# Kernel optimization log

Hardware: AMD Instinct MI355X
Metric: run time of the kernel (lower is better)

## Reference

```python
import jax, jax.numpy as jnp
import numpy as np

B, L, HID = 2, 2048, 512
NUM_HEADS = 8
HEAD_DIM = HID // NUM_HEADS
GAP_ROWS = 33   # num_time_gap_buckets + 1
DUR_ROWS = 17   # num_duration_buckets + 1
NEG = -1e9      # finite stand-in for -inf (grad-safe, masked probs ~0)


def setup_inputs() -> dict:
    key = jax.random.key(0)
    ks = jax.random.split(key, 16)
    s = 1.0 / np.sqrt(HID)
    x = jax.random.normal(ks[0], (B, L, HID), dtype=jnp.float32)
    attention_mask = jax.random.randint(ks[1], (B, L), 0, 2, dtype=jnp.int32)
    time_gap_bucket_ids = jax.random.randint(ks[2], (B, L), 0, GAP_ROWS, dtype=jnp.int32)
    duration_bucket_ids = jax.random.randint(ks[3], (B, L), 0, DUR_ROWS, dtype=jnp.int32)
    Wq = jax.random.normal(ks[4], (HID, HID), dtype=jnp.float32) * s
    bq = jnp.zeros((HID,), jnp.float32)
    Wk = jax.random.normal(ks[5], (HID, HID), dtype=jnp.float32) * s
    bk = jnp.zeros((HID,), jnp.float32)
    Wv = jax.random.normal(ks[6], (HID, HID), dtype=jnp.float32) * s
    bv = jnp.zeros((HID,), jnp.float32)
    Wo = jax.random.normal(ks[7], (HID, HID), dtype=jnp.float32) * s
    bo = jnp.zeros((HID,), jnp.float32)
    # bias tables: padding_idx=0 row kept at zero, rest random for a meaningful test
    gap_emb = jax.random.normal(ks[8], (GAP_ROWS, NUM_HEADS), dtype=jnp.float32) * 0.1
    gap_emb = gap_emb.at[0].set(0.0)
    dur_emb = jax.random.normal(ks[9], (DUR_ROWS, NUM_HEADS), dtype=jnp.float32) * 0.1
    dur_emb = dur_emb.at[0].set(0.0)
    return dict(x=x, attention_mask=attention_mask,
                time_gap_bucket_ids=time_gap_bucket_ids,
                duration_bucket_ids=duration_bucket_ids,
                Wq=Wq, bq=bq, Wk=Wk, bk=bk, Wv=Wv, bv=bv, Wo=Wo, bo=bo,
                gap_emb=gap_emb, dur_emb=dur_emb)


def reference(x, attention_mask, time_gap_bucket_ids, duration_bucket_ids,
              Wq, bq, Wk, bk, Wv, bv, Wo, bo, gap_emb, dur_emb):
    b, l, hid = x.shape
    h, d = NUM_HEADS, HEAD_DIM
    def split_heads(t):  # (B,L,HID) -> (B,h,L,d)
        return t.reshape(b, l, h, d).transpose(0, 2, 1, 3)
    Q = split_heads(x @ Wq + bq)
    K = split_heads(x @ Wk + bk)
    V = split_heads(x @ Wv + bv)
    scores = jnp.einsum('bhqd,bhkd->bhqk', Q, K) / jnp.sqrt(jnp.float32(d))
    # relative time-gap bias: (B,L,L) bucket lookup -> (B,h,L,L)
    rel = jnp.abs(time_gap_bucket_ids[:, :, None] - time_gap_bucket_ids[:, None, :])
    rel = jnp.clip(rel, 0, GAP_ROWS - 1)
    gap_bias = gap_emb[rel]                       # (B,L,L,h)
    scores = scores + gap_bias.transpose(0, 3, 1, 2)
    # per-key duration bias: (B,L,h) -> (B,h,1,L)
    dur_bias = dur_emb[duration_bucket_ids]       # (B,L,h)
    scores = scores + dur_bias.transpose(0, 2, 1)[:, :, None, :]
    pad = (attention_mask == 0)[:, None, None, :]  # (B,1,1,L) over keys
    scores = jnp.where(pad, NEG, scores)
    attn = jax.nn.softmax(scores, axis=-1)
    out = jnp.einsum('bhqk,bhkd->bhqd', attn, V)
    out = out.transpose(0, 2, 1, 3).reshape(b, l, hid)
    return out @ Wo + bo
```

## Files before the change

kernel.cpp:

```cpp
#include <hip/hip_runtime.h>
#include <cmath>

typedef unsigned short u16;
typedef unsigned int   u32;
typedef __attribute__((ext_vector_type(2))) unsigned uintx2;
typedef __attribute__((ext_vector_type(4))) float    floatx4;
typedef __attribute__((ext_vector_type(4))) unsigned uintx4;
typedef __attribute__((ext_vector_type(8))) __bf16   bf16x8;

#define MFMA16(a, b, c) __builtin_amdgcn_mfma_f32_16x16x32_bf16((a), (b), (c), 0, 0, 0)

__device__ __forceinline__ u16 f2bf(float f) {
    union { float f; u32 u; } v; v.f = f;
    u32 u = v.u;
    return (u16)((u + 0x7FFFu + ((u >> 16) & 1u)) >> 16);
}

__device__ __forceinline__ bf16x8 ld_frag(const u16* p) {
    uintx4 t = *(const uintx4*)p;
    return __builtin_bit_cast(bf16x8, t);
}

#if __has_builtin(__builtin_amdgcn_exp2f)
#define EXP2F(x) __builtin_amdgcn_exp2f(x)
#else
#define EXP2F(x) exp2f(x)
#endif

typedef __attribute__((address_space(3))) unsigned       lds_u32;
typedef __attribute__((address_space(1))) const unsigned glb_u32;
__device__ __forceinline__ void gl_lds16(const void* g, void* l) {
    __builtin_amdgcn_global_load_lds((glb_u32*)(uintptr_t)g, (lds_u32*)(uintptr_t)l, 16, 0, 0);
}

#define LOG2E   1.4426950408889634f
#define QSCALE  0.18033688011112043f

__global__ __launch_bounds__(256) void cast_x_kernel(const float* __restrict__ x,
                                                     u16* __restrict__ Xb) {
    int idx = blockIdx.x * 256 + threadIdx.x;
    const float* src = x + (size_t)idx * 8;
    uintx4 o;
    o.x = f2bf(src[0]) | ((u32)f2bf(src[1]) << 16);
    o.y = f2bf(src[2]) | ((u32)f2bf(src[3]) << 16);
    o.z = f2bf(src[4]) | ((u32)f2bf(src[5]) << 16);
    o.w = f2bf(src[6]) | ((u32)f2bf(src[7]) << 16);
    *(uintx4*)(Xb + (size_t)idx * 8) = o;
}

__global__ __launch_bounds__(256) void transpose_w_kernel(
        const float* __restrict__ Wq, const float* __restrict__ Wk,
        const float* __restrict__ Wv, const float* __restrict__ Wo,
        u16* __restrict__ WqT, u16* __restrict__ WkT,
        u16* __restrict__ WvT, u16* __restrict__ WoT) {
    int m = blockIdx.y;
    const float* W = (m == 0) ? Wq : (m == 1) ? Wk : (m == 2) ? Wv : Wo;
    u16* WT = (m == 0) ? WqT : (m == 1) ? WkT : (m == 2) ? WvT : WoT;
    int idx = blockIdx.x * 256 + threadIdx.x;
    int n = idx >> 9, k = idx & 511;
    WT[idx] = f2bf(W[(size_t)k * 512 + n]);
}

__global__ __launch_bounds__(256) void ext_q_kernel(const int* __restrict__ gap_ids,
                                                    u16* __restrict__ Qe) {
    int idx = blockIdx.x * 256 + threadIdx.x;
    int bh = idx >> 11, l = idx & 2047;
    int b = bh >> 3;
    int gq = gap_ids[b * 2048 + l];
    u16 lg = f2bf(LOG2E);
    u16* dst = Qe + (size_t)idx * 128;
    for (int ch = 8; ch < 16; ch++) {
        u16 vals[8];
        for (int e = 0; e < 8; e++) {
            int j = (ch - 8) * 8 + e;
            vals[e] = (j == gq || j == 33) ? lg : (u16)0;
        }
        *(uintx4*)(dst + ch * 8) = *(uintx4*)vals;
    }
}

__global__ __launch_bounds__(256) void ext_k_kernel(const int* __restrict__ gap_ids,
                                                    const int* __restrict__ dur_ids,
                                                    const int* __restrict__ amask,
                                                    const float* __restrict__ gap_emb,
                                                    const float* __restrict__ dur_emb,
                                                    u16* __restrict__ Ke) {
    int idx = blockIdx.x * 256 + threadIdx.x;
    int bh = idx >> 11, l = idx & 2047;
    int b = bh >> 3, h = bh & 7;
    int gk = gap_ids[b * 2048 + l];
    int did = dur_ids[b * 2048 + l];
    int msk = amask[b * 2048 + l];
    float kval = msk ? dur_emb[did * 8 + h] : -1e9f;
    u16* dst = Ke + (size_t)idx * 128;
    int sw = l & 7;
    for (int ch = 8; ch < 16; ch++) {
        u16 vals[8];
        for (int e = 0; e < 8; e++) {
            int j = (ch - 8) * 8 + e;
            float v;
            if (j <= 32) { int d = j - gk; d = d < 0 ? -d : d; v = gap_emb[d * 8 + h]; }
            else if (j == 33) v = kval;
            else v = 0.f;
            vals[e] = f2bf(v);
        }
        int phys = 8 | ((ch & 7) ^ sw);
        *(uintx4*)(dst + phys * 8) = *(uintx4*)vals;
    }
}

__global__ __launch_bounds__(256) void gemm_qkv(
        const u16* __restrict__ Xb,
        const u16* __restrict__ WqT, const u16* __restrict__ WkT, const u16* __restrict__ WvT,
        const float* __restrict__ bq, const float* __restrict__ bk, const float* __restrict__ bv,
        u16* __restrict__ Qe, u16* __restrict__ Ke, u16* __restrict__ Vt) {
    __shared__ u16 As[64][72];
    __shared__ u16 Bs[64][72];
    int tid = threadIdx.x;
    int m0 = blockIdx.x * 64;
    int n0 = blockIdx.y * 64;
    int mat = n0 >> 9;
    int ncol0 = n0 & 511;
    const u16* Bt = (mat == 0) ? WqT : (mat == 1) ? WkT : WvT;
    const float* bias = (mat == 0) ? bq : (mat == 1) ? bk : bv;

    int lane = tid & 63, w = tid >> 6, lo = lane & 15, hi = lane >> 4;
    floatx4 acc[4] = {};

    for (int kb = 0; kb < 8; kb++) {
        __syncthreads();
        for (int c = tid; c < 512; c += 256) {
            int row = c >> 3, cc = c & 7;
            *(uintx4*)&As[row][cc * 8] =
                *(const uintx4*)&Xb[(size_t)(m0 + row) * 512 + kb * 64 + cc * 8];
            *(uintx4*)&Bs[row][cc * 8] =
                *(const uintx4*)&Bt[(size_t)(ncol0 + row) * 512 + kb * 64 + cc * 8];
        }
        __syncthreads();
        for (int s = 0; s < 2; s++) {
            bf16x8 a = ld_frag(&As[16 * w + lo][8 * hi + 32 * s]);
            for (int t = 0; t < 4; t++) {
                bf16x8 b = ld_frag(&Bs[16 * t + lo][8 * hi + 32 * s]);
                acc[t] = MFMA16(a, b, acc[t]);
            }
        }
    }

    int h = ncol0 >> 6;
    for (int t = 0; t < 4; t++) {
        int dc = 16 * t + lo;
        float bval = bias[ncol0 + dc];
        for (int r = 0; r < 4; r++) {
            int mrow = m0 + 16 * w + 4 * hi + r;
            int bb = mrow >> 11, lrow = mrow & 2047;
            float v = acc[t][r] + bval;
            size_t rowi = (size_t)(bb * 8 + h) * 2048 + lrow;
            if (mat == 0) {
                Qe[rowi * 128 + dc] = f2bf(v * QSCALE);
            } else if (mat == 1) {
                int phys = (((dc >> 3) ^ (lrow & 7)) << 3) | (dc & 7);
                Ke[rowi * 128 + phys] = f2bf(v);
            } else {
                int kl = lrow & 63;
                int cl = kl >> 2, e2 = kl & 3;
                int pos = (lrow & ~63) | (((cl ^ (dc & 15)) << 2) | e2);
                Vt[((size_t)(bb * 8 + h) * 64 + dc) * 2048 + pos] = f2bf(v);
            }
        }
    }
}

__global__ __launch_bounds__(256, 6) void flash_attn(
        const u16* __restrict__ Qe, const u16* __restrict__ Ke, const u16* __restrict__ Vt,
        float* __restrict__ Opart, float* __restrict__ Lpart) {
    __shared__ u16 Ks[64 * 128];
    __shared__ u16 Vs[64 * 64];

    int tid = threadIdx.x, lane = tid & 63, w = tid >> 6, lo = lane & 15, hi = lane >> 4;
    int qt = blockIdx.x, bh = blockIdx.y, sp = blockIdx.z;
    int q0 = qt * 64;
    int sw = lo & 7;

    size_t qrow = ((size_t)bh * 2048 + q0 + 16 * w + lo) * 128;
    bf16x8 bq_[4];
    for (int kc = 0; kc < 4; kc++) bq_[kc] = ld_frag(&Qe[qrow + kc * 32 + hi * 8]);

    floatx4 O[4] = {};
    float l_acc = 0.f;
    const u16* KeB = Ke + (size_t)bh * 2048 * 128;
    const u16* VtB = Vt + (size_t)bh * 64 * 2048;

    int kbeg = (sp * 32) / 3, kend = ((sp + 1) * 32) / 3;
    for (int kt = kbeg; kt < kend; kt++) {
        int k0 = kt * 64;
        __syncthreads();
        {
            const char* g = (const char*)(KeB + (size_t)k0 * 128);
            char* l = (char*)Ks;
            for (int r2 = 0; r2 < 4; r2++)
                gl_lds16(g + r2 * 4096 + tid * 16, l + r2 * 4096 + tid * 16);
        }
        {
            for (int p2 = 0; p2 < 2; p2++) {
                int c = p2 * 256 + tid;
                int row = c >> 3, ch = c & 7;
                const char* g = (const char*)(VtB + (size_t)row * 2048 + k0) + ch * 16;
                gl_lds16(g, (char*)Vs + c * 16);
            }
        }
        __syncthreads();

        floatx4 sf[4] = {};
        for (int t = 0; t < 4; t++) {
            const u16* krow = &Ks[(16 * t + lo) * 128];
            for (int kc = 0; kc < 4; kc++) {
                int cc = kc * 4 + hi;
                int pc = (cc & 8) | ((cc & 7) ^ sw);
                bf16x8 a = ld_frag(&krow[pc * 8]);
                sf[t] = MFMA16(a, bq_[kc], sf[t]);
            }
        }

        u32 pk[4][2];
        for (int t = 0; t < 4; t++) {
            float p0 = EXP2F(sf[t][0]);
            float p1 = EXP2F(sf[t][1]);
            float p2 = EXP2F(sf[t][2]);
            float p3 = EXP2F(sf[t][3]);
            l_acc += (p0 + p1) + (p2 + p3);
            u32 u0 = __builtin_bit_cast(u32, p0) + 0x8000u;
            u32 u1 = __builtin_bit_cast(u32, p1) + 0x8000u;
            u32 u2 = __builtin_bit_cast(u32, p2) + 0x8000u;
            u32 u3 = __builtin_bit_cast(u32, p3) + 0x8000u;
            pk[t][0] = __builtin_amdgcn_perm(u1, u0, 0x07060302);
            pk[t][1] = __builtin_amdgcn_perm(u3, u2, 0x07060302);
        }

        for (int tp = 0; tp < 2; tp++) {
            uintx4 av;
            av.x = pk[2 * tp][0]; av.y = pk[2 * tp][1];
            av.z = pk[2 * tp + 1][0]; av.w = pk[2 * tp + 1][1];
            bf16x8 af = __builtin_bit_cast(bf16x8, av);
            for (int u = 0; u < 4; u++) {
                const u16* vrow = &Vs[(16 * u + lo) * 64];
                int c0 = (8 * tp + hi) ^ lo;
                int c1 = (8 * tp + 4 + hi) ^ lo;
                uintx2 lo64 = *(const uintx2*)&vrow[c0 * 4];
                uintx2 hi64 = *(const uintx2*)&vrow[c1 * 4];
                uintx4 bv;
                bv.x = lo64.x; bv.y = lo64.y; bv.z = hi64.x; bv.w = hi64.y;
                O[u] = MFMA16(af, __builtin_bit_cast(bf16x8, bv), O[u]);
            }
        }
    }

    l_acc += __shfl_xor(l_acc, 16);
    l_acc += __shfl_xor(l_acc, 32);

    size_t obase = (((size_t)sp * 16 + bh) * 32 + qt) * 4096;
    for (int u = 0; u < 4; u++)
        for (int r = 0; r < 4; r++)
            Opart[obase + (size_t)(16 * w + 4 * hi + r) * 64 + 16 * u + lo] = O[u][r];
    if (hi == 0)
        Lpart[(((size_t)sp * 16 + bh) * 32 + qt) * 64 + 16 * w + lo] = l_acc;
}

__global__ __launch_bounds__(256) void combine_kernel(const float* __restrict__ Opart,
                                                      const float* __restrict__ Lpart,
                                                      u16* __restrict__ Ob) {
    int idx = blockIdx.x * 256 + threadIdx.x;
    int d = idx & 63;
    int q = (idx >> 6) & 2047;
    int bh = idx >> 17;
    int qt = q >> 6, qr = q & 63;
    size_t b0 = ((size_t)bh * 32 + qt) * 4096 + qr * 64 + d;
    float o = Opart[b0] + Opart[b0 + 2097152] + Opart[b0 + 2 * 2097152];
    size_t lb = ((size_t)bh * 32 + qt) * 64 + qr;
    float l = Lpart[lb] + Lpart[lb + 32768] + Lpart[lb + 2 * 32768];
    int bb = bh >> 3, h = bh & 7;
    Ob[((size_t)(bb * 2048 + q)) * 512 + h * 64 + d] = f2bf(o / l);
}

__global__ __launch_bounds__(256) void gemm_out(
        const u16* __restrict__ Ob, const u16* __restrict__ WoT,
        const float* __restrict__ bo, float* __restrict__ out) {
    __shared__ u16 As[64][72];
    __shared__ u16 Bs[64][72];
    int tid = threadIdx.x;
    int m0 = blockIdx.x * 64;
    int n0 = blockIdx.y * 64;
    int lane = tid & 63, w = tid >> 6, lo = lane & 15, hi = lane >> 4;
    floatx4 acc[4] = {};

    for (int kb = 0; kb < 8; kb++) {
        __syncthreads();
        for (int c = tid; c < 512; c += 256) {
            int row = c >> 3, cc = c & 7;
            *(uintx4*)&As[row][cc * 8] =
                *(const uintx4*)&Ob[(size_t)(m0 + row) * 512 + kb * 64 + cc * 8];
            *(uintx4*)&Bs[row][cc * 8] =
                *(const uintx4*)&WoT[(size_t)(n0 + row) * 512 + kb * 64 + cc * 8];
        }
        __syncthreads();
        for (int s = 0; s < 2; s++) {
            bf16x8 a = ld_frag(&As[16 * w + lo][8 * hi + 32 * s]);
            for (int t = 0; t < 4; t++) {
                bf16x8 b = ld_frag(&Bs[16 * t + lo][8 * hi + 32 * s]);
                acc[t] = MFMA16(a, b, acc[t]);
            }
        }
    }
    for (int t = 0; t < 4; t++) {
        int n = n0 + 16 * t + lo;
        float bval = bo[n];
        for (int r = 0; r < 4; r++) {
            int mrow = m0 + 16 * w + 4 * hi + r;
            out[(size_t)mrow * 512 + n] = acc[t][r] + bval;
        }
    }
}

extern "C" void kernel_launch(void* const* d_in, const int* in_sizes, int n_in,
                              void* d_out, int out_size, void* d_ws, size_t ws_size,
                              hipStream_t stream) {
    const float* x     = (const float*)d_in[0];
    const int*   amask = (const int*)d_in[1];
    const int*   gids  = (const int*)d_in[2];
    const int*   dids  = (const int*)d_in[3];
    const float* Wq    = (const float*)d_in[4];
    const float* bq    = (const float*)d_in[5];
    const float* Wk    = (const float*)d_in[6];
    const float* bk    = (const float*)d_in[7];
    const float* Wv    = (const float*)d_in[8];
    const float* bv    = (const float*)d_in[9];
    const float* Wo    = (const float*)d_in[10];
    const float* bo    = (const float*)d_in[11];
    const float* gap_emb = (const float*)d_in[12];
    const float* dur_emb = (const float*)d_in[13];
    float* out = (float*)d_out;

    char* ws = (char*)d_ws;
    u16*   Qe    = (u16*)(ws + 0);
    u16*   Ke    = (u16*)(ws + 8388608);
    u16*   Vt    = (u16*)(ws + 16777216);
    float* Opart = (float*)(ws + 20971520);
    float* Lpart = (float*)(ws + 46137344);
    u16*   Ob    = (u16*)(ws + 46530560);
    u16*   WoT   = (u16*)(ws + 50724864);
    u16*   Xb    = (u16*)(ws + 20971520);
    u16*   WqT   = (u16*)(ws + 25165824);
    u16*   WkT   = (u16*)(ws + 25690112);
    u16*   WvT   = (u16*)(ws + 26214400);

    hipLaunchKernelGGL(cast_x_kernel, dim3(1024), dim3(256), 0, stream, x, Xb);
    hipLaunchKernelGGL(transpose_w_kernel, dim3(1024, 4), dim3(256), 0, stream,
                       Wq, Wk, Wv, Wo, WqT, WkT, WvT, WoT);
    hipLaunchKernelGGL(gemm_qkv, dim3(64, 24), dim3(256), 0, stream,
                       Xb, WqT, WkT, WvT, bq, bk, bv, Qe, Ke, Vt);
    hipLaunchKernelGGL(ext_q_kernel, dim3(128), dim3(256), 0, stream, gids, Qe);
    hipLaunchKernelGGL(ext_k_kernel, dim3(128), dim3(256), 0, stream,
                       gids, dids, amask, gap_emb, dur_emb, Ke);
    hipLaunchKernelGGL(flash_attn, dim3(32, 16, 3), dim3(256), 0, stream,
                       Qe, Ke, Vt, Opart, Lpart);
    hipLaunchKernelGGL(combine_kernel, dim3(8192), dim3(256), 0, stream,
                       Opart, Lpart, Ob);
    hipLaunchKernelGGL(gemm_out, dim3(64, 8), dim3(256), 0, stream,
                       Ob, WoT, bo, out);
}
```

Baseline: 175.9 us.

## Fuse prep kernels, enlarge GEMM tiles, MFMA row-sums, vectorize combine and transpose

Merges the x cast and the Q/K extension-column kernels into one prep launch that runs before the QKV GEMM, removing two launches. The weight transpose becomes an LDS-tiled transpose with coalesced loads and stores. Both GEMMs move to 128x128 tiles with a 2x2 wave layout and global_load_lds staging, which raises data reuse per block but also raises register and LDS use. Flash attention computes the softmax denominator with an MFMA against a ones vector instead of scalar adds and shuffles, and the combine kernel handles four outputs per thread with vector loads.

```diff
diff --git a/kernel.cpp b/kernel.cpp
--- a/kernel.cpp
+++ b/kernel.cpp
@@ -36,16 +36,60 @@
 #define LOG2E   1.4426950408889634f
 #define QSCALE  0.18033688011112043f
 
-__global__ __launch_bounds__(256) void cast_x_kernel(const float* __restrict__ x,
-                                                     u16* __restrict__ Xb) {
-    int idx = blockIdx.x * 256 + threadIdx.x;
-    const float* src = x + (size_t)idx * 8;
-    uintx4 o;
-    o.x = f2bf(src[0]) | ((u32)f2bf(src[1]) << 16);
-    o.y = f2bf(src[2]) | ((u32)f2bf(src[3]) << 16);
-    o.z = f2bf(src[4]) | ((u32)f2bf(src[5]) << 16);
-    o.w = f2bf(src[6]) | ((u32)f2bf(src[7]) << 16);
-    *(uintx4*)(Xb + (size_t)idx * 8) = o;
+__global__ __launch_bounds__(256) void prep_kernel(
+        const float* __restrict__ x, const int* __restrict__ gap_ids,
+        const int* __restrict__ dur_ids, const int* __restrict__ amask,
+        const float* __restrict__ gap_emb, const float* __restrict__ dur_emb,
+        u16* __restrict__ Xb, u16* __restrict__ Qe, u16* __restrict__ Ke) {
+    int bid = blockIdx.x, tid = threadIdx.x;
+    if (bid < 1024) {
+        int idx = bid * 256 + tid;
+        const float* src = x + (size_t)idx * 8;
+        uintx4 o;
+        o.x = f2bf(src[0]) | ((u32)f2bf(src[1]) << 16);
+        o.y = f2bf(src[2]) | ((u32)f2bf(src[3]) << 16);
+        o.z = f2bf(src[4]) | ((u32)f2bf(src[5]) << 16);
+        o.w = f2bf(src[6]) | ((u32)f2bf(src[7]) << 16);
+        *(uintx4*)(Xb + (size_t)idx * 8) = o;
+    } else if (bid < 1152) {
+        int idx = (bid - 1024) * 256 + tid;
+        int l = idx & 2047;
+        int b = idx >> 14;
+        int gq = gap_ids[b * 2048 + l];
+        u16 lg = f2bf(LOG2E);
+        u16* dst = Qe + (size_t)idx * 128;
+        for (int ch = 8; ch < 16; ch++) {
+            u16 vals[8];
+            for (int e = 0; e < 8; e++) {
+                int j = (ch - 8) * 8 + e;
+                vals[e] = (j == gq || j == 33) ? lg : (u16)0;
+            }
+            *(uintx4*)(dst + ch * 8) = *(uintx4*)vals;
+        }
+    } else {
+        int idx = (bid - 1152) * 256 + tid;
+        int bh = idx >> 11, l = idx & 2047;
+        int b = bh >> 3, h = bh & 7;
+        int gk = gap_ids[b * 2048 + l];
+        int did = dur_ids[b * 2048 + l];
+        int msk = amask[b * 2048 + l];
+        float kval = msk ? dur_emb[did * 8 + h] : -1e9f;
+        u16* dst = Ke + (size_t)idx * 128;
+        int sw = l & 7;
+        for (int ch = 8; ch < 16; ch++) {
+            u16 vals[8];
+            for (int e = 0; e < 8; e++) {
+                int j = (ch - 8) * 8 + e;
+                float v;
+                if (j <= 32) { int d = j - gk; d = d < 0 ? -d : d; v = gap_emb[d * 8 + h]; }
+                else if (j == 33) v = kval;
+                else v = 0.f;
+                vals[e] = f2bf(v);
+            }
+            int phys = 8 | ((ch & 7) ^ sw);
+            *(uintx4*)(dst + phys * 8) = *(uintx4*)vals;
+        }
+    }
 }
 
 __global__ __launch_bounds__(256) void transpose_w_kernel(
@@ -53,59 +97,26 @@
         const float* __restrict__ Wv, const float* __restrict__ Wo,
         u16* __restrict__ WqT, u16* __restrict__ WkT,
         u16* __restrict__ WvT, u16* __restrict__ WoT) {
-    int m = blockIdx.y;
-    const float* W = (m == 0) ? Wq : (m == 1) ? Wk : (m == 2) ? Wv : Wo;
-    u16* WT = (m == 0) ? WqT : (m == 1) ? WkT : (m == 2) ? WvT : WoT;
-    int idx = blockIdx.x * 256 + threadIdx.x;
-    int n = idx >> 9, k = idx & 511;
-    WT[idx] = f2bf(W[(size_t)k * 512 + n]);
-}
-
-__global__ __launch_bounds__(256) void ext_q_kernel(const int* __restrict__ gap_ids,
-                                                    u16* __restrict__ Qe) {
-    int idx = blockIdx.x * 256 + threadIdx.x;
-    int bh = idx >> 11, l = idx & 2047;
-    int b = bh >> 3;
-    int gq = gap_ids[b * 2048 + l];
-    u16 lg = f2bf(LOG2E);
-    u16* dst = Qe + (size_t)idx * 128;
-    for (int ch = 8; ch < 16; ch++) {
-        u16 vals[8];
-        for (int e = 0; e < 8; e++) {
-            int j = (ch - 8) * 8 + e;
-            vals[e] = (j == gq || j == 33) ? lg : (u16)0;
-        }
-        *(uintx4*)(dst + ch * 8) = *(uintx4*)vals;
-    }
-}
-
-__global__ __launch_bounds__(256) void ext_k_kernel(const int* __restrict__ gap_ids,
-                                                    const int* __restrict__ dur_ids,
-                                                    const int* __restrict__ amask,
-                                                    const float* __restrict__ gap_emb,
-                                                    const float* __restrict__ dur_emb,
-                                                    u16* __restrict__ Ke) {
-    int idx = blockIdx.x * 256 + threadIdx.x;
-    int bh = idx >> 11, l = idx & 2047;
-    int b = bh >> 3, h = bh & 7;
-    int gk = gap_ids[b * 2048 + l];
-    int did = dur_ids[b * 2048 + l];
-    int msk = amask[b * 2048 + l];
-    float kval = msk ? dur_emb[did * 8 + h] : -1e9f;
-    u16* dst = Ke + (size_t)idx * 128;
-    int sw = l & 7;
-    for (int ch = 8; ch < 16; ch++) {
-        u16 vals[8];
-        for (int e = 0; e < 8; e++) {
-            int j = (ch - 8) * 8 + e;
-            float v;
-            if (j <= 32) { int d = j - gk; d = d < 0 ? -d : d; v = gap_emb[d * 8 + h]; }
-            else if (j == 33) v = kval;
-            else v = 0.f;
-            vals[e] = f2bf(v);
-        }
-        int phys = 8 | ((ch & 7) ^ sw);
-        *(uintx4*)(dst + phys * 8) = *(uintx4*)vals;
+    __shared__ u16 T[64][72];
+    int bid = blockIdx.x, tid = threadIdx.x;
+    int mat = bid >> 6, t8 = bid & 63;
+    int n0 = (t8 & 7) * 64, k0 = (t8 >> 3) * 64;
+    const float* W = (mat == 0) ? Wq : (mat == 1) ? Wk : (mat == 2) ? Wv : Wo;
+    u16* WT = (mat == 0) ? WqT : (mat == 1) ? WkT : (mat == 2) ? WvT : WoT;
+    int r = tid >> 4, cq = tid & 15;
+    for (int rr = 0; rr < 4; rr++) {
+        int row = r + rr * 16;
+        floatx4 s = *(const floatx4*)&W[(size_t)(k0 + row) * 512 + n0 + cq * 4];
+        T[cq * 4 + 0][row] = f2bf(s.x);
+        T[cq * 4 + 1][row] = f2bf(s.y);
+        T[cq * 4 + 2][row] = f2bf(s.z);
+        T[cq * 4 + 3][row] = f2bf(s.w);
+    }
+    __syncthreads();
+    for (int p = 0; p < 2; p++) {
+        int idx = p * 256 + tid;
+        int c = idx >> 3, ch = idx & 7;
+        *(uintx4*)&WT[(size_t)(n0 + c) * 512 + k0 + ch * 8] = *(const uintx4*)&T[c][ch * 8];
     }
 }
 
@@ -114,59 +125,69 @@
         const u16* __restrict__ WqT, const u16* __restrict__ WkT, const u16* __restrict__ WvT,
         const float* __restrict__ bq, const float* __restrict__ bk, const float* __restrict__ bv,
         u16* __restrict__ Qe, u16* __restrict__ Ke, u16* __restrict__ Vt) {
-    __shared__ u16 As[64][72];
-    __shared__ u16 Bs[64][72];
+    __shared__ u16 As[128 * 64];
+    __shared__ u16 Bs[128 * 64];
     int tid = threadIdx.x;
-    int m0 = blockIdx.x * 64;
-    int n0 = blockIdx.y * 64;
-    int mat = n0 >> 9;
-    int ncol0 = n0 & 511;
+    int m0 = blockIdx.x * 128;
+    int gy = blockIdx.y;
+    int mat = gy >> 2;
+    int ncol0 = (gy & 3) * 128;
     const u16* Bt = (mat == 0) ? WqT : (mat == 1) ? WkT : WvT;
     const float* bias = (mat == 0) ? bq : (mat == 1) ? bk : bv;
 
     int lane = tid & 63, w = tid >> 6, lo = lane & 15, hi = lane >> 4;
-    floatx4 acc[4] = {};
+    int wm = w >> 1, wn = w & 1;
+    floatx4 acc[4][4] = {};
 
     for (int kb = 0; kb < 8; kb++) {
-        __syncthreads();
-        for (int c = tid; c < 512; c += 256) {
-            int row = c >> 3, cc = c & 7;
-            *(uintx4*)&As[row][cc * 8] =
-                *(const uintx4*)&Xb[(size_t)(m0 + row) * 512 + kb * 64 + cc * 8];
-            *(uintx4*)&Bs[row][cc * 8] =
-                *(const uintx4*)&Bt[(size_t)(ncol0 + row) * 512 + kb * 64 + cc * 8];
+        int k0 = kb * 64;
+        __syncthreads();
+        for (int it = 0; it < 4; it++) {
+            int c = it * 256 + tid;
+            int row = c >> 3, ch = c & 7;
+            gl_lds16((const char*)Xb + ((size_t)(m0 + row) * 512 + k0) * 2 + ch * 16,
+                     (char*)As + c * 16);
+        }
+        for (int it = 0; it < 4; it++) {
+            int c = it * 256 + tid;
+            int row = c >> 3, ch = c & 7;
+            gl_lds16((const char*)Bt + ((size_t)(ncol0 + row) * 512 + k0) * 2 + ch * 16,
+                     (char*)Bs + c * 16);
         }
         __syncthreads();
         for (int s = 0; s < 2; s++) {
-            bf16x8 a = ld_frag(&As[16 * w + lo][8 * hi + 32 * s]);
-            for (int t = 0; t < 4; t++) {
-                bf16x8 b = ld_frag(&Bs[16 * t + lo][8 * hi + 32 * s]);
-                acc[t] = MFMA16(a, b, acc[t]);
-            }
-        }
-    }
-
-    int h = ncol0 >> 6;
-    for (int t = 0; t < 4; t++) {
-        int dc = 16 * t + lo;
-        float bval = bias[ncol0 + dc];
-        for (int r = 0; r < 4; r++) {
-            int mrow = m0 + 16 * w + 4 * hi + r;
-            int bb = mrow >> 11, lrow = mrow & 2047;
-            float v = acc[t][r] + bval;
-            size_t rowi = (size_t)(bb * 8 + h) * 2048 + lrow;
-            if (mat == 0) {
-                Qe[rowi * 128 + dc] = f2bf(v * QSCALE);
-            } else if (mat == 1) {
-                int phys = (((dc >> 3) ^ (lrow & 7)) << 3) | (dc & 7);
-                Ke[rowi * 128 + phys] = f2bf(v);
-            } else {
-                int kl = lrow & 63;
-                int cl = kl >> 2, e2 = kl & 3;
-                int pos = (lrow & ~63) | (((cl ^ (dc & 15)) << 2) | e2);
-                Vt[((size_t)(bb * 8 + h) * 64 + dc) * 2048 + pos] = f2bf(v);
-            }
-        }
+            bf16x8 a[4], b[4];
+            for (int i = 0; i < 4; i++)
+                a[i] = ld_frag(&As[(64 * wm + 16 * i + lo) * 64 + s * 32 + hi * 8]);
+            for (int j = 0; j < 4; j++)
+                b[j] = ld_frag(&Bs[(64 * wn + 16 * j + lo) * 64 + s * 32 + hi * 8]);
+            for (int i = 0; i < 4; i++)
+                for (int j = 0; j < 4; j++)
+                    acc[i][j] = MFMA16(a[i], b[j], acc[i][j]);
+        }
+    }
+
+    for (int j = 0; j < 4; j++) {
+        int col = ncol0 + 64 * wn + 16 * j + lo;
+        float bval = bias[col];
+        int h = col >> 6, dc = col & 63;
+        for (int i = 0; i < 4; i++)
+            for (int r = 0; r < 4; r++) {
+                int mrow = m0 + 64 * wm + 16 * i + 4 * hi + r;
+                int bb = mrow >> 11, lrow = mrow & 2047;
+                float v = acc[i][j][r] + bval;
+                size_t rowi = (size_t)(bb * 8 + h) * 2048 + lrow;
+                if (mat == 0) {
+                    Qe[rowi * 128 + dc] = f2bf(v * QSCALE);
+                } else if (mat == 1) {
+                    int phys = (((dc >> 3) ^ (lrow & 7)) << 3) | (dc & 7);
+                    Ke[rowi * 128 + phys] = f2bf(v);
+                } else {
+                    int kl = lrow & 63, cl = kl >> 2, e2 = kl & 3;
+                    int pos = (lrow & ~63) | ((cl ^ (dc & 15)) << 2) | e2;
+                    Vt[((size_t)(bb * 8 + h) * 64 + dc) * 2048 + pos] = f2bf(v);
+                }
+            }
     }
 }
 
@@ -186,7 +207,10 @@
     for (int kc = 0; kc < 4; kc++) bq_[kc] = ld_frag(&Qe[qrow + kc * 32 + hi * 8]);
 
     floatx4 O[4] = {};
-    float l_acc = 0.f;
+    floatx4 Lacc = {};
+    uintx4 onesu; onesu.x = 0x3F803F80u; onesu.y = 0x3F803F80u; onesu.z = 0x3F803F80u; onesu.w = 0x3F803F80u;
+    bf16x8 ones = __builtin_bit_cast(bf16x8, onesu);
+
     const u16* KeB = Ke + (size_t)bh * 2048 * 128;
     const u16* VtB = Vt + (size_t)bh * 64 * 2048;
 
@@ -227,7 +251,6 @@
             float p1 = EXP2F(sf[t][1]);
             float p2 = EXP2F(sf[t][2]);
             float p3 = EXP2F(sf[t][3]);
-            l_acc += (p0 + p1) + (p2 + p3);
             u32 u0 = __builtin_bit_cast(u32, p0) + 0x8000u;
             u32 u1 = __builtin_bit_cast(u32, p1) + 0x8000u;
             u32 u2 = __builtin_bit_cast(u32, p2) + 0x8000u;
@@ -241,6 +264,7 @@
             av.x = pk[2 * tp][0]; av.y = pk[2 * tp][1];
             av.z = pk[2 * tp + 1][0]; av.w = pk[2 * tp + 1][1];
             bf16x8 af = __builtin_bit_cast(bf16x8, av);
+            Lacc = MFMA16(af, ones, Lacc);
             for (int u = 0; u < 4; u++) {
                 const u16* vrow = &Vs[(16 * u + lo) * 64];
                 int c0 = (8 * tp + hi) ^ lo;
@@ -254,69 +278,85 @@
         }
     }
 
-    l_acc += __shfl_xor(l_acc, 16);
-    l_acc += __shfl_xor(l_acc, 32);
-
     size_t obase = (((size_t)sp * 16 + bh) * 32 + qt) * 4096;
     for (int u = 0; u < 4; u++)
         for (int r = 0; r < 4; r++)
             Opart[obase + (size_t)(16 * w + 4 * hi + r) * 64 + 16 * u + lo] = O[u][r];
-    if (hi == 0)
-        Lpart[(((size_t)sp * 16 + bh) * 32 + qt) * 64 + 16 * w + lo] = l_acc;
+    if (lo == 0) {
+        size_t lbase = (((size_t)sp * 16 + bh) * 32 + qt) * 64;
+        for (int r = 0; r < 4; r++) Lpart[lbase + 16 * w + 4 * hi + r] = Lacc[r];
+    }
 }
 
 __global__ __launch_bounds__(256) void combine_kernel(const float* __restrict__ Opart,
                                                       const float* __restrict__ Lpart,
                                                       u16* __restrict__ Ob) {
     int idx = blockIdx.x * 256 + threadIdx.x;
-    int d = idx & 63;
-    int q = (idx >> 6) & 2047;
-    int bh = idx >> 17;
+    int d4 = idx & 15;
+    int q = (idx >> 4) & 2047;
+    int bh = idx >> 15;
     int qt = q >> 6, qr = q & 63;
-    size_t b0 = ((size_t)bh * 32 + qt) * 4096 + qr * 64 + d;
-    float o = Opart[b0] + Opart[b0 + 2097152] + Opart[b0 + 2 * 2097152];
+    size_t b0 = ((size_t)bh * 32 + qt) * 4096 + qr * 64 + d4 * 4;
+    floatx4 o0 = *(const floatx4*)&Opart[b0];
+    floatx4 o1 = *(const floatx4*)&Opart[b0 + 2097152];
+    floatx4 o2 = *(const floatx4*)&Opart[b0 + 4194304];
     size_t lb = ((size_t)bh * 32 + qt) * 64 + qr;
-    float l = Lpart[lb] + Lpart[lb + 32768] + Lpart[lb + 2 * 32768];
+    float rl = 1.0f / (Lpart[lb] + Lpart[lb + 32768] + Lpart[lb + 65536]);
+    uintx2 pk2;
+    pk2.x = f2bf((o0.x + o1.x + o2.x) * rl) | ((u32)f2bf((o0.y + o1.y + o2.y) * rl) << 16);
+    pk2.y = f2bf((o0.z + o1.z + o2.z) * rl) | ((u32)f2bf((o0.w + o1.w + o2.w) * rl) << 16);
     int bb = bh >> 3, h = bh & 7;
-    Ob[((size_t)(bb * 2048 + q)) * 512 + h * 64 + d] = f2bf(o / l);
+    *(uintx2*)&Ob[((size_t)(bb * 2048 + q)) * 512 + h * 64 + d4 * 4] = pk2;
 }
 
 __global__ __launch_bounds__(256) void gemm_out(
         const u16* __restrict__ Ob, const u16* __restrict__ WoT,
         const float* __restrict__ bo, float* __restrict__ out) {
-    __shared__ u16 As[64][72];
-    __shared__ u16 Bs[64][72];
+    __shared__ u16 As[128 * 64];
+    __shared__ u16 Bs[128 * 64];
     int tid = threadIdx.x;
-    int m0 = blockIdx.x * 64;
-    int n0 = blockIdx.y * 64;
+    int m0 = blockIdx.x * 128;
+    int n0 = blockIdx.y * 128;
     int lane = tid & 63, w = tid >> 6, lo = lane & 15, hi = lane >> 4;
-    floatx4 acc[4] = {};
+    int wm = w >> 1, wn = w & 1;
+    floatx4 acc[4][4] = {};
 
     for (int kb = 0; kb < 8; kb++) {
-        __syncthreads();
-        for (int c = tid; c < 512; c += 256) {
-            int row = c >> 3, cc = c & 7;
-            *(uintx4*)&As[row][cc * 8] =
-                *(const uintx4*)&Ob[(size_t)(m0 + row) * 512 + kb * 64 + cc * 8];
-            *(uintx4*)&Bs[row][cc * 8] =
-                *(const uintx4*)&WoT[(size_t)(n0 + row) * 512 + kb * 64 + cc * 8];
+        int k0 = kb * 64;
+        __syncthreads();
+        for (int it = 0; it < 4; it++) {
+            int c = it * 256 + tid;
+            int row = c >> 3, ch = c & 7;
+            gl_lds16((const char*)Ob + ((size_t)(m0 + row) * 512 + k0) * 2 + ch * 16,
+                     (char*)As + c * 16);
+        }
+        for (int it = 0; it < 4; it++) {
+            int c = it * 256 + tid;
+            int row = c >> 3, ch = c & 7;
+            gl_lds16((const char*)WoT + ((size_t)(n0 + row) * 512 + k0) * 2 + ch * 16,
+                     (char*)Bs + c * 16);
         }
         __syncthreads();
         for (int s = 0; s < 2; s++) {
-            bf16x8 a = ld_frag(&As[16 * w + lo][8 * hi + 32 * s]);
-            for (int t = 0; t < 4; t++) {
-                bf16x8 b = ld_frag(&Bs[16 * t + lo][8 * hi + 32 * s]);
-                acc[t] = MFMA16(a, b, acc[t]);
-            }
-        }
-    }
-    for (int t = 0; t < 4; t++) {
-        int n = n0 + 16 * t + lo;
-        float bval = bo[n];
-        for (int r = 0; r < 4; r++) {
-            int mrow = m0 + 16 * w + 4 * hi + r;
-            out[(size_t)mrow * 512 + n] = acc[t][r] + bval;
-        }
+            bf16x8 a[4], b[4];
+            for (int i = 0; i < 4; i++)
+                a[i] = ld_frag(&As[(64 * wm + 16 * i + lo) * 64 + s * 32 + hi * 8]);
+            for (int j = 0; j < 4; j++)
+                b[j] = ld_frag(&Bs[(64 * wn + 16 * j + lo) * 64 + s * 32 + hi * 8]);
+            for (int i = 0; i < 4; i++)
+                for (int j = 0; j < 4; j++)
+                    acc[i][j] = MFMA16(a[i], b[j], acc[i][j]);
+        }
+    }
+
+    for (int j = 0; j < 4; j++) {
+        int col = n0 + 64 * wn + 16 * j + lo;
+        float bval = bo[col];
+        for (int i = 0; i < 4; i++)
+            for (int r = 0; r < 4; r++) {
+                int mrow = m0 + 64 * wm + 16 * i + 4 * hi + r;
+                out[(size_t)mrow * 512 + col] = acc[i][j][r] + bval;
+            }
     }
 }
 
@@ -352,18 +392,16 @@
     u16*   WkT   = (u16*)(ws + 25690112);
     u16*   WvT   = (u16*)(ws + 26214400);
 
-    hipLaunchKernelGGL(cast_x_kernel, dim3(1024), dim3(256), 0, stream, x, Xb);
-    hipLaunchKernelGGL(transpose_w_kernel, dim3(1024, 4), dim3(256), 0, stream,
+    hipLaunchKernelGGL(prep_kernel, dim3(1280), dim3(256), 0, stream,
+                       x, gids, dids, amask, gap_emb, dur_emb, Xb, Qe, Ke);
+    hipLaunchKernelGGL(transpose_w_kernel, dim3(256), dim3(256), 0, stream,
                        Wq, Wk, Wv, Wo, WqT, WkT, WvT, WoT);
-    hipLaunchKernelGGL(gemm_qkv, dim3(64, 24), dim3(256), 0, stream,
+    hipLaunchKernelGGL(gemm_qkv, dim3(32, 12), dim3(256), 0, stream,
                        Xb, WqT, WkT, WvT, bq, bk, bv, Qe, Ke, Vt);
-    hipLaunchKernelGGL(ext_q_kernel, dim3(128), dim3(256), 0, stream, gids, Qe);
-    hipLaunchKernelGGL(ext_k_kernel, dim3(128), dim3(256), 0, stream,
-                       gids, dids, amask, gap_emb, dur_emb, Ke);
     hipLaunchKernelGGL(flash_attn, dim3(32, 16, 3), dim3(256), 0, stream,
                        Qe, Ke, Vt, Opart, Lpart);
-    hipLaunchKernelGGL(combine_kernel, dim3(8192), dim3(256), 0, stream,
+    hipLaunchKernelGGL(combine_kernel, dim3(2048), dim3(256), 0, stream,
                        Opart, Lpart, Ob);
-    hipLaunchKernelGGL(gemm_out, dim3(64, 8), dim3(256), 0, stream,
+    hipLaunchKernelGGL(gemm_out, dim3(32, 4), dim3(256), 0, stream,
                        Ob, WoT, bo, out);
 }
```

After: 250.6 us. 1.42x slower.
